# Kernel tuning notes

Hardware: AMD Instinct MI355X
Metric: run time of the kernel (lower is better)

The kernel has to match this reference:

```python
import jax, jax.numpy as jnp
import numpy as np

BERT_DIM = 768
N_ROWS = 5
N_COLS = 12
LN_EPS = 1e-5


def setup_inputs() -> dict:
    key = jax.random.key(0)
    ks = jax.random.split(key, 12)
    B, S = 256, 512
    token_hidden = jax.random.normal(ks[0], (B, S, BERT_DIM), dtype=jnp.float32)
    attention_mask = jax.random.randint(ks[1], (B, S), 0, 2, dtype=jnp.int32)
    s = lambda fan_in: 1.0 / np.sqrt(fan_in)
    return {
        "token_hidden": token_hidden,
        "attention_mask": attention_mask,
        # token_attention: Linear(768,128) -> Tanh -> Linear(128,1)
        "att_w1": jax.random.normal(ks[2], (128, BERT_DIM), dtype=jnp.float32) * s(BERT_DIM),
        "att_b1": jnp.zeros((128,), dtype=jnp.float32),
        "att_w2": jax.random.normal(ks[3], (1, 128), dtype=jnp.float32) * s(128),
        "att_b2": jnp.zeros((1,), dtype=jnp.float32),
        # feature_projector: Linear(768,256) -> GELU -> Dropout(eval) -> Linear(256,5)
        "proj_w1": jax.random.normal(ks[4], (256, BERT_DIM), dtype=jnp.float32) * s(BERT_DIM),
        "proj_b1": jnp.zeros((256,), dtype=jnp.float32),
        "proj_w2": jax.random.normal(ks[5], (N_ROWS, 256), dtype=jnp.float32) * s(256),
        "proj_b2": jnp.zeros((N_ROWS,), dtype=jnp.float32),
        # LayerNorm([5, 12])
        "ln_gamma": jnp.ones((N_ROWS, N_COLS), dtype=jnp.float32),
        "ln_beta": jnp.zeros((N_ROWS, N_COLS), dtype=jnp.float32),
    }


def reference(token_hidden, attention_mask, att_w1, att_b1, att_w2, att_b2,
              proj_w1, proj_b1, proj_w2, proj_b2, ln_gamma, ln_beta):
    # token attention scores: [B, S]
    h = jnp.tanh(jnp.einsum("bsd,hd->bsh", token_hidden, att_w1) + att_b1)
    scores = (jnp.einsum("bsh,oh->bso", h, att_w2) + att_b2)[..., 0]
    scores = jnp.where(attention_mask == 0, jnp.finfo(scores.dtype).min, scores)
    weights = jax.nn.softmax(scores, axis=-1)
    # top-k token selection (indices sorted ascending to preserve order)
    k = min(N_COLS, token_hidden.shape[1])
    _, top_idx = jax.lax.top_k(weights, k)  # [B, k]
    top_idx = jnp.sort(top_idx, axis=-1)
    selected = jnp.take_along_axis(token_hidden, top_idx[:, :, None], axis=1)  # [B, k, D]
    # feature projector (dropout is eval no-op)
    f = jax.nn.gelu(jnp.einsum("bkd,hd->bkh", selected, proj_w1) + proj_b1, approximate=False)
    f = jnp.einsum("bkh,rh->bkr", f, proj_w2) + proj_b2  # [B, k, n_rows]
    features = jnp.transpose(f, (0, 2, 1))  # [B, n_rows, k]
    if features.shape[-1] < N_COLS:
        features = jnp.pad(features, ((0, 0), (0, 0), (0, N_COLS - features.shape[-1])))
    # LayerNorm over trailing [n_rows, n_cols]
    mean = jnp.mean(features, axis=(-2, -1), keepdims=True)
    var = jnp.var(features, axis=(-2, -1), keepdims=True)
    return ln_gamma * (features - mean) * jax.lax.rsqrt(var + LN_EPS) + ln_beta
```

## Files before the change

kernel.cpp:

```cpp
#include <hip/hip_runtime.h>
#include <math.h>

#define B_BATCH 256
#define S_LEN   512
#define D_DIM   768
#define H_ATT   128
#define TOPK    12
#define NCAND   16
#define H_PROJ  256
#define N_ROWS  5
#define N_COLS  12

typedef __bf16 bf16x8 __attribute__((ext_vector_type(8)));
typedef float  f32x4  __attribute__((ext_vector_type(4)));

#define WS_SCORES 0
#define WS_WHI    524288
#define WS_WLO    720896
#define WS_W1Q    917504
#define WS_W1P    1310720

__global__ __launch_bounds__(256) void prep_kernel(
    const float* __restrict__ w1,
    const float* __restrict__ pw1,
    __bf16* __restrict__ whi, __bf16* __restrict__ wlo,
    float* __restrict__ w1q, float* __restrict__ w1p)
{
    int id = blockIdx.x * 256 + threadIdx.x;
    if (id < 98304) {
        int j    = id & 7;
        int lane = (id >> 3) & 63;
        int rest = id >> 9;
        int nt   = rest & 7;
        int kt   = rest >> 3;
        int n = nt * 16 + (lane & 15);
        int k = kt * 32 + (lane >> 4) * 8 + j;
        float f = w1[n * D_DIM + k];
        __bf16 h = (__bf16)f;
        whi[id] = h;
        wlo[id] = (__bf16)(f - (float)h);
    } else if (id < 196608) {
        int e2 = id - 98304;
        int i  = e2 & 3;
        int n  = (e2 >> 2) & 127;
        int k4 = e2 >> 9;
        w1q[e2] = w1[n * D_DIM + k4 * 4 + i];
    } else {
        int e  = id - 196608;
        int i  = e & 3;
        int j  = (e >> 2) & 255;
        int k4 = e >> 10;
        w1p[e] = pw1[j * D_DIM + k4 * 4 + i];
    }
}

__device__ inline void split8(float4 a, float4 b, bf16x8& hi, bf16x8& lo) {
    float v[8] = {a.x, a.y, a.z, a.w, b.x, b.y, b.z, b.w};
#pragma unroll
    for (int i = 0; i < 8; ++i) {
        __bf16 h = (__bf16)v[i];
        hi[i] = h;
        lo[i] = (__bf16)(v[i] - (float)h);
    }
}

__global__ __launch_bounds__(256, 3) void score_mfma(
    const float*  __restrict__ th,
    const __bf16* __restrict__ whi,
    const __bf16* __restrict__ wlo,
    const float*  __restrict__ b1,
    const float*  __restrict__ w2,
    float* __restrict__ scores)
{
    const int tid = threadIdx.x;
    const int wv  = tid >> 6;
    const int ln  = tid & 63;

    const size_t row0 = (size_t)blockIdx.x * 128 + wv * 32 + (ln & 15);
    const float* pa0 = th + row0 * D_DIM + (ln >> 4) * 8;
    const float* pa1 = pa0 + 16 * D_DIM;

    f32x4 acc[2][8];
    const f32x4 z = {0.f, 0.f, 0.f, 0.f};
#pragma unroll
    for (int i = 0; i < 2; ++i)
#pragma unroll
        for (int j = 0; j < 8; ++j) acc[i][j] = z;

    float4 c00 = *(const float4*)(pa0);
    float4 c01 = *(const float4*)(pa0 + 4);
    float4 c10 = *(const float4*)(pa1);
    float4 c11 = *(const float4*)(pa1 + 4);

    for (int kt = 0; kt < 24; ++kt) {
        float4 n00, n01, n10, n11;
        if (kt < 23) {
            n00 = *(const float4*)(pa0 + (kt + 1) * 32);
            n01 = *(const float4*)(pa0 + (kt + 1) * 32 + 4);
            n10 = *(const float4*)(pa1 + (kt + 1) * 32);
            n11 = *(const float4*)(pa1 + (kt + 1) * 32 + 4);
        }

        bf16x8 ah0, al0, ah1, al1;
        split8(c00, c01, ah0, al0);
        split8(c10, c11, ah1, al1);

        const __bf16* ph = whi + (size_t)kt * 4096 + (size_t)ln * 8;
        const __bf16* pl = wlo + (size_t)kt * 4096 + (size_t)ln * 8;
#pragma unroll
        for (int nt = 0; nt < 8; ++nt) {
            bf16x8 bh = *(const bf16x8*)(ph + nt * 512);
            bf16x8 bl = *(const bf16x8*)(pl + nt * 512);
            acc[0][nt] = __builtin_amdgcn_mfma_f32_16x16x32_bf16(ah0, bh, acc[0][nt], 0, 0, 0);
            acc[0][nt] = __builtin_amdgcn_mfma_f32_16x16x32_bf16(al0, bh, acc[0][nt], 0, 0, 0);
            acc[0][nt] = __builtin_amdgcn_mfma_f32_16x16x32_bf16(ah0, bl, acc[0][nt], 0, 0, 0);
            acc[1][nt] = __builtin_amdgcn_mfma_f32_16x16x32_bf16(ah1, bh, acc[1][nt], 0, 0, 0);
            acc[1][nt] = __builtin_amdgcn_mfma_f32_16x16x32_bf16(al1, bh, acc[1][nt], 0, 0, 0);
            acc[1][nt] = __builtin_amdgcn_mfma_f32_16x16x32_bf16(ah1, bl, acc[1][nt], 0, 0, 0);
        }
        if (kt < 23) {
            c00 = n00; c01 = n01; c10 = n10; c11 = n11;
        }
    }

    const int col = ln & 15;
    float b1v[8], w2v[8];
#pragma unroll
    for (int nt = 0; nt < 8; ++nt) {
        b1v[nt] = b1[nt * 16 + col];
        w2v[nt] = w2[nt * 16 + col];
    }
    const size_t rowbase = (size_t)blockIdx.x * 128 + wv * 32;
#pragma unroll
    for (int mf = 0; mf < 2; ++mf)
#pragma unroll
        for (int r = 0; r < 4; ++r) {
            float s = 0.f;
#pragma unroll
            for (int nt = 0; nt < 8; ++nt)
                s += tanhf(acc[mf][nt][r] + b1v[nt]) * w2v[nt];
            s += __shfl_xor(s, 1, 64);
            s += __shfl_xor(s, 2, 64);
            s += __shfl_xor(s, 4, 64);
            s += __shfl_xor(s, 8, 64);
            if (col == 0)
                scores[rowbase + mf * 16 + (ln >> 4) * 4 + r] = s;
        }
}

__global__ __launch_bounds__(256) void select_kernel(
    const float* __restrict__ th,
    const int*   __restrict__ mask,
    const float* __restrict__ ascores,
    const float* __restrict__ w1q,
    const float* __restrict__ ab1,
    const float* __restrict__ aw2,
    const float* __restrict__ w1p,
    const float* __restrict__ pb1,
    const float* __restrict__ pw2,
    const float* __restrict__ pb2,
    const float* __restrict__ gamma,
    const float* __restrict__ beta,
    float* __restrict__ out)
{
    const int b   = blockIdx.x;
    const int tid = threadIdx.x;
    const int wv  = tid >> 6;
    const int ln  = tid & 63;

    __shared__ float4 xc[NCAND][192];
    __shared__ unsigned long long wtop[64];
    __shared__ int   cand[NCAND];
    __shared__ float redW[4][8];
    __shared__ float exact_sc[NCAND];
    __shared__ int   sel_slot[TOPK];
    __shared__ float gbuf[TOPK][H_PROJ + 4];
    __shared__ float feat[N_ROWS * N_COLS];
    __shared__ float stats[2];

    const float NEG_MIN = -3.402823466e38f;

    {
        int i0 = wv * 128 + ln, i1 = i0 + 64;
        float v0 = ascores[(size_t)b * S_LEN + i0];
        if (mask[(size_t)b * S_LEN + i0] == 0) v0 = NEG_MIN;
        float v1 = ascores[(size_t)b * S_LEN + i1];
        if (mask[(size_t)b * S_LEN + i1] == 0) v1 = NEG_MIN;
        unsigned k0 = __float_as_uint(v0);
        k0 = ((int)k0 >= 0) ? (k0 | 0x80000000u) : ~k0;
        unsigned k1 = __float_as_uint(v1);
        k1 = ((int)k1 >= 0) ? (k1 | 0x80000000u) : ~k1;
        unsigned long long p0 = ((unsigned long long)k0 << 32) | (0xFFFFFFFFu - (unsigned)i0);
        unsigned long long p1 = ((unsigned long long)k1 << 32) | (0xFFFFFFFFu - (unsigned)i1);
        for (int it = 0; it < NCAND; ++it) {
            unsigned long long m = p0 > p1 ? p0 : p1;
#pragma unroll
            for (int s = 1; s <= 32; s <<= 1) {
                unsigned long long o = __shfl_xor(m, s, 64);
                if (o > m) m = o;
            }
            if (ln == 0) wtop[wv * 16 + it] = m;
            if (p0 == m) p0 = 0ull;
            else if (p1 == m) p1 = 0ull;
        }
    }
    __syncthreads();
    if (wv == 0) {
        unsigned long long q = wtop[ln];
        for (int it = 0; it < NCAND; ++it) {
            unsigned long long m = q;
#pragma unroll
            for (int s = 1; s <= 32; s <<= 1) {
                unsigned long long o = __shfl_xor(m, s, 64);
                if (o > m) m = o;
            }
            if (ln == 0) cand[it] = (int)(0xFFFFFFFFu - (unsigned)(m & 0xFFFFFFFFu));
            if (q == m) q = 0ull;
        }
    }
    __syncthreads();

#pragma unroll
    for (int i = 0; i < 12; ++i) {
        int f = tid + 256 * i;
        int c = f / 192, k4 = f % 192;
        xc[c][k4] = *(const float4*)(th + ((size_t)b * S_LEN + cand[c]) * D_DIM + k4 * 4);
    }
    __syncthreads();

    {
        const int n = tid & 127;
        const int h = tid >> 7;
        float accs[8];
#pragma unroll
        for (int ci = 0; ci < 8; ++ci) accs[ci] = 0.f;
        for (int k4 = 0; k4 < 192; ++k4) {
            float4 w = *(const float4*)(w1q + (size_t)(k4 * 128 + n) * 4);
#pragma unroll
            for (int ci = 0; ci < 8; ++ci) {
                float4 x = xc[2 * ci + h][k4];
                accs[ci] += w.x * x.x + w.y * x.y + w.z * x.z + w.w * x.w;
            }
        }
        float b1n = ab1[n], w2n = aw2[n];
#pragma unroll
        for (int ci = 0; ci < 8; ++ci) {
            float val = tanhf(accs[ci] + b1n) * w2n;
            val += __shfl_xor(val, 1, 64);
            val += __shfl_xor(val, 2, 64);
            val += __shfl_xor(val, 4, 64);
            val += __shfl_xor(val, 8, 64);
            val += __shfl_xor(val, 16, 64);
            val += __shfl_xor(val, 32, 64);
            if (ln == 0) redW[wv][ci] = val;
        }
    }
    __syncthreads();
    if (tid < NCAND) {
        int c = tid;
        float ex = (c & 1) ? (redW[2][c >> 1] + redW[3][c >> 1])
                           : (redW[0][c >> 1] + redW[1][c >> 1]);
        if (mask[(size_t)b * S_LEN + cand[c]] == 0) ex = -INFINITY;
        exact_sc[c] = ex;
    }
    __syncthreads();

    if (tid == 0) {
        unsigned picked = 0;
        int slots[TOPK];
        for (int it = 0; it < TOPK; ++it) {
            float best = -INFINITY; int bslot = -1; int bidx = 1 << 30;
            for (int c = 0; c < NCAND; ++c) {
                if (picked & (1u << c)) continue;
                float e = exact_sc[c]; int idx = cand[c];
                if (e > best || (e == best && idx < bidx)) { best = e; bslot = c; bidx = idx; }
            }
            picked |= 1u << bslot;
            slots[it] = bslot;
        }
        for (int i = 1; i < TOPK; ++i) {
            int s = slots[i], key = cand[s], j = i - 1;
            while (j >= 0 && cand[slots[j]] > key) { slots[j + 1] = slots[j]; --j; }
            slots[j + 1] = s;
        }
        for (int t = 0; t < TOPK; ++t) sel_slot[t] = slots[t];
    }
    __syncthreads();

    {
        const int j = tid;
        int slots[TOPK];
#pragma unroll
        for (int t = 0; t < TOPK; ++t) slots[t] = sel_slot[t];
        float accp[TOPK];
        float bj = pb1[j];
#pragma unroll
        for (int t = 0; t < TOPK; ++t) accp[t] = bj;
        for (int k4 = 0; k4 < 192; ++k4) {
            float4 w = *(const float4*)(w1p + ((size_t)k4 * 256 + j) * 4);
#pragma unroll
            for (int t = 0; t < TOPK; ++t) {
                float4 x = xc[slots[t]][k4];
                accp[t] += w.x * x.x + w.y * x.y + w.z * x.z + w.w * x.w;
            }
        }
#pragma unroll
        for (int t = 0; t < TOPK; ++t) {
            float hh = accp[t];
            gbuf[t][j] = 0.5f * hh * (1.0f + erff(hh * 0.70710678118654752f));
        }
    }
    __syncthreads();

    if (tid < TOPK * N_ROWS) {
        int t = tid / N_ROWS, r = tid % N_ROWS;
        float s = pb2[r];
        const float4* gp = (const float4*)&gbuf[t][0];
        const float4* wp = (const float4*)(pw2 + r * H_PROJ);
        for (int q = 0; q < H_PROJ / 4; ++q) {
            float4 g = gp[q], w = wp[q];
            s += g.x * w.x + g.y * w.y + g.z * w.z + g.w * w.w;
        }
        feat[r * N_COLS + t] = s;
    }
    __syncthreads();

    if (tid == 0) {
        float sum = 0.f;
        for (int i = 0; i < N_ROWS * N_COLS; ++i) sum += feat[i];
        float mean = sum / 60.f;
        float sq = 0.f;
        for (int i = 0; i < N_ROWS * N_COLS; ++i) { float d = feat[i] - mean; sq += d * d; }
        stats[0] = mean;
        stats[1] = sq / 60.f;
    }
    __syncthreads();
    if (tid < N_ROWS * N_COLS) {
        float x = feat[tid];
        out[(size_t)b * 60 + tid] =
            gamma[tid] * (x - stats[0]) * rsqrtf(stats[1] + 1e-5f) + beta[tid];
    }
}

extern "C" void kernel_launch(void* const* d_in, const int* in_sizes, int n_in,
                              void* d_out, int out_size, void* d_ws, size_t ws_size,
                              hipStream_t stream) {
    const float* th   = (const float*)d_in[0];
    const int*   mask = (const int*)  d_in[1];
    const float* aw1  = (const float*)d_in[2];
    const float* ab1  = (const float*)d_in[3];
    const float* aw2  = (const float*)d_in[4];
    const float* pw1  = (const float*)d_in[6];
    const float* pb1  = (const float*)d_in[7];
    const float* pw2  = (const float*)d_in[8];
    const float* pb2  = (const float*)d_in[9];
    const float* gam  = (const float*)d_in[10];
    const float* bet  = (const float*)d_in[11];
    float* out = (float*)d_out;

    char* ws = (char*)d_ws;
    float*  scores = (float*)(ws + WS_SCORES);
    __bf16* whi    = (__bf16*)(ws + WS_WHI);
    __bf16* wlo    = (__bf16*)(ws + WS_WLO);
    float*  w1q    = (float*)(ws + WS_W1Q);
    float*  w1p    = (float*)(ws + WS_W1P);

    hipLaunchKernelGGL(prep_kernel, dim3(1536), dim3(256), 0, stream,
                       aw1, pw1, whi, wlo, w1q, w1p);
    hipLaunchKernelGGL(score_mfma, dim3(1024), dim3(256), 0, stream,
                       th, whi, wlo, ab1, aw2, scores);
    hipLaunchKernelGGL(select_kernel, dim3(B_BATCH), dim3(256), 0, stream,
                       th, mask, scores, w1q, ab1, aw2,
                       w1p, pb1, pw2, pb2, gam, bet, out);
}
```

Baseline: 752.7 us.

## Stage split-bf16 weight tiles into double-buffered LDS via global_load_lds

The score kernel now loads the hi/lo bf16 weight fragments once per block into a double-buffered shared-memory tile using direct global-to-LDS loads, with the next k-tile prefetched while the current one is consumed. Previously each of the four waves read the same weight fragments separately from global memory. The prep kernel's weight layout is reordered to nt-major so each staged chunk is contiguous. The cost is a block-wide barrier per k-step and 32KB of LDS, which may limit occupancy under the 3-blocks launch bound.

```diff
diff --git a/kernel.cpp b/kernel.cpp
--- a/kernel.cpp
+++ b/kernel.cpp
@@ -13,6 +13,9 @@
 
 typedef __bf16 bf16x8 __attribute__((ext_vector_type(8)));
 typedef float  f32x4  __attribute__((ext_vector_type(4)));
+
+#define GLOBAL_AS __attribute__((address_space(1)))
+#define LDS_AS    __attribute__((address_space(3)))
 
 #define WS_SCORES 0
 #define WS_WHI    524288
@@ -31,8 +34,8 @@
         int j    = id & 7;
         int lane = (id >> 3) & 63;
         int rest = id >> 9;
-        int nt   = rest & 7;
-        int kt   = rest >> 3;
+        int kt   = rest % 24;
+        int nt   = rest / 24;
         int n = nt * 16 + (lane & 15);
         int k = kt * 32 + (lane >> 4) * 8 + j;
         float f = w1[n * D_DIM + k];
@@ -72,6 +75,8 @@
     const float*  __restrict__ w2,
     float* __restrict__ scores)
 {
+    __shared__ __bf16 Bs[2][2][8 * 512];
+
     const int tid = threadIdx.x;
     const int wv  = tid >> 6;
     const int ln  = tid & 63;
@@ -79,6 +84,20 @@
     const size_t row0 = (size_t)blockIdx.x * 128 + wv * 32 + (ln & 15);
     const float* pa0 = th + row0 * D_DIM + (ln >> 4) * 8;
     const float* pa1 = pa0 + 16 * D_DIM;
+
+    auto stage = [&](int kt, int buf) {
+#pragma unroll
+        for (int q = 0; q < 4; ++q) {
+            int s  = wv + q * 4;
+            int hl = s >> 3;
+            int nt = s & 7;
+            const __bf16* src = (hl ? wlo : whi) +
+                                (((size_t)nt * 24 + kt) * 64 + ln) * 8;
+            __bf16* dst = &Bs[buf][hl][nt * 512];
+            __builtin_amdgcn_global_load_lds(
+                (GLOBAL_AS const void*)src, (LDS_AS void*)dst, 16, 0, 0);
+        }
+    };
 
     f32x4 acc[2][8];
     const f32x4 z = {0.f, 0.f, 0.f, 0.f};
@@ -91,26 +110,28 @@
     float4 c01 = *(const float4*)(pa0 + 4);
     float4 c10 = *(const float4*)(pa1);
     float4 c11 = *(const float4*)(pa1 + 4);
+    stage(0, 0);
+    __syncthreads();
 
     for (int kt = 0; kt < 24; ++kt) {
+        const int buf = kt & 1;
         float4 n00, n01, n10, n11;
         if (kt < 23) {
             n00 = *(const float4*)(pa0 + (kt + 1) * 32);
             n01 = *(const float4*)(pa0 + (kt + 1) * 32 + 4);
             n10 = *(const float4*)(pa1 + (kt + 1) * 32);
             n11 = *(const float4*)(pa1 + (kt + 1) * 32 + 4);
+            stage(kt + 1, buf ^ 1);
         }
 
         bf16x8 ah0, al0, ah1, al1;
         split8(c00, c01, ah0, al0);
         split8(c10, c11, ah1, al1);
 
-        const __bf16* ph = whi + (size_t)kt * 4096 + (size_t)ln * 8;
-        const __bf16* pl = wlo + (size_t)kt * 4096 + (size_t)ln * 8;
 #pragma unroll
         for (int nt = 0; nt < 8; ++nt) {
-            bf16x8 bh = *(const bf16x8*)(ph + nt * 512);
-            bf16x8 bl = *(const bf16x8*)(pl + nt * 512);
+            bf16x8 bh = *(bf16x8*)(&Bs[buf][0][nt * 512 + ln * 8]);
+            bf16x8 bl = *(bf16x8*)(&Bs[buf][1][nt * 512 + ln * 8]);
             acc[0][nt] = __builtin_amdgcn_mfma_f32_16x16x32_bf16(ah0, bh, acc[0][nt], 0, 0, 0);
             acc[0][nt] = __builtin_amdgcn_mfma_f32_16x16x32_bf16(al0, bh, acc[0][nt], 0, 0, 0);
             acc[0][nt] = __builtin_amdgcn_mfma_f32_16x16x32_bf16(ah0, bl, acc[0][nt], 0, 0, 0);
@@ -120,6 +141,7 @@
         }
         if (kt < 23) {
             c00 = n00; c01 = n01; c10 = n10; c11 = n11;
+            __syncthreads();
         }
     }
 
```

New measurement: 726.1 us. 1.04x faster.

## Fuse score GEMM, top-k selection and projection into one per-batch kernel

Applied to the files above, without the earlier changes.

Removes the weight prep kernel and the separate MFMA score kernel, and computes attention scores inside a single per-batch kernel with 512 threads that keeps scores in shared memory. Weights are now read in their original row-major layout and split into bf16 hi/lo inside the MFMA loop, instead of being pre-swizzled. This drops two launches and the global round trip for scores. In exchange only 256 blocks run the heavy score GEMM (fewer blocks than the previous 1024), weight loads become strided and uncoalesced, and the per-iteration weight splitting adds ALU work and register pressure.

```diff
diff --git a/kernel.cpp b/kernel.cpp
--- a/kernel.cpp
+++ b/kernel.cpp
@@ -14,46 +14,6 @@
 typedef __bf16 bf16x8 __attribute__((ext_vector_type(8)));
 typedef float  f32x4  __attribute__((ext_vector_type(4)));
 
-#define WS_SCORES 0
-#define WS_WHI    524288
-#define WS_WLO    720896
-#define WS_W1Q    917504
-#define WS_W1P    1310720
-
-__global__ __launch_bounds__(256) void prep_kernel(
-    const float* __restrict__ w1,
-    const float* __restrict__ pw1,
-    __bf16* __restrict__ whi, __bf16* __restrict__ wlo,
-    float* __restrict__ w1q, float* __restrict__ w1p)
-{
-    int id = blockIdx.x * 256 + threadIdx.x;
-    if (id < 98304) {
-        int j    = id & 7;
-        int lane = (id >> 3) & 63;
-        int rest = id >> 9;
-        int nt   = rest & 7;
-        int kt   = rest >> 3;
-        int n = nt * 16 + (lane & 15);
-        int k = kt * 32 + (lane >> 4) * 8 + j;
-        float f = w1[n * D_DIM + k];
-        __bf16 h = (__bf16)f;
-        whi[id] = h;
-        wlo[id] = (__bf16)(f - (float)h);
-    } else if (id < 196608) {
-        int e2 = id - 98304;
-        int i  = e2 & 3;
-        int n  = (e2 >> 2) & 127;
-        int k4 = e2 >> 9;
-        w1q[e2] = w1[n * D_DIM + k4 * 4 + i];
-    } else {
-        int e  = id - 196608;
-        int i  = e & 3;
-        int j  = (e >> 2) & 255;
-        int k4 = e >> 10;
-        w1p[e] = pw1[j * D_DIM + k4 * 4 + i];
-    }
-}
-
 __device__ inline void split8(float4 a, float4 b, bf16x8& hi, bf16x8& lo) {
     float v[8] = {a.x, a.y, a.z, a.w, b.x, b.y, b.z, b.w};
 #pragma unroll
@@ -64,98 +24,13 @@
     }
 }
 
-__global__ __launch_bounds__(256, 3) void score_mfma(
-    const float*  __restrict__ th,
-    const __bf16* __restrict__ whi,
-    const __bf16* __restrict__ wlo,
-    const float*  __restrict__ b1,
-    const float*  __restrict__ w2,
-    float* __restrict__ scores)
-{
-    const int tid = threadIdx.x;
-    const int wv  = tid >> 6;
-    const int ln  = tid & 63;
-
-    const size_t row0 = (size_t)blockIdx.x * 128 + wv * 32 + (ln & 15);
-    const float* pa0 = th + row0 * D_DIM + (ln >> 4) * 8;
-    const float* pa1 = pa0 + 16 * D_DIM;
-
-    f32x4 acc[2][8];
-    const f32x4 z = {0.f, 0.f, 0.f, 0.f};
-#pragma unroll
-    for (int i = 0; i < 2; ++i)
-#pragma unroll
-        for (int j = 0; j < 8; ++j) acc[i][j] = z;
-
-    float4 c00 = *(const float4*)(pa0);
-    float4 c01 = *(const float4*)(pa0 + 4);
-    float4 c10 = *(const float4*)(pa1);
-    float4 c11 = *(const float4*)(pa1 + 4);
-
-    for (int kt = 0; kt < 24; ++kt) {
-        float4 n00, n01, n10, n11;
-        if (kt < 23) {
-            n00 = *(const float4*)(pa0 + (kt + 1) * 32);
-            n01 = *(const float4*)(pa0 + (kt + 1) * 32 + 4);
-            n10 = *(const float4*)(pa1 + (kt + 1) * 32);
-            n11 = *(const float4*)(pa1 + (kt + 1) * 32 + 4);
-        }
-
-        bf16x8 ah0, al0, ah1, al1;
-        split8(c00, c01, ah0, al0);
-        split8(c10, c11, ah1, al1);
-
-        const __bf16* ph = whi + (size_t)kt * 4096 + (size_t)ln * 8;
-        const __bf16* pl = wlo + (size_t)kt * 4096 + (size_t)ln * 8;
-#pragma unroll
-        for (int nt = 0; nt < 8; ++nt) {
-            bf16x8 bh = *(const bf16x8*)(ph + nt * 512);
-            bf16x8 bl = *(const bf16x8*)(pl + nt * 512);
-            acc[0][nt] = __builtin_amdgcn_mfma_f32_16x16x32_bf16(ah0, bh, acc[0][nt], 0, 0, 0);
-            acc[0][nt] = __builtin_amdgcn_mfma_f32_16x16x32_bf16(al0, bh, acc[0][nt], 0, 0, 0);
-            acc[0][nt] = __builtin_amdgcn_mfma_f32_16x16x32_bf16(ah0, bl, acc[0][nt], 0, 0, 0);
-            acc[1][nt] = __builtin_amdgcn_mfma_f32_16x16x32_bf16(ah1, bh, acc[1][nt], 0, 0, 0);
-            acc[1][nt] = __builtin_amdgcn_mfma_f32_16x16x32_bf16(al1, bh, acc[1][nt], 0, 0, 0);
-            acc[1][nt] = __builtin_amdgcn_mfma_f32_16x16x32_bf16(ah1, bl, acc[1][nt], 0, 0, 0);
-        }
-        if (kt < 23) {
-            c00 = n00; c01 = n01; c10 = n10; c11 = n11;
-        }
-    }
-
-    const int col = ln & 15;
-    float b1v[8], w2v[8];
-#pragma unroll
-    for (int nt = 0; nt < 8; ++nt) {
-        b1v[nt] = b1[nt * 16 + col];
-        w2v[nt] = w2[nt * 16 + col];
-    }
-    const size_t rowbase = (size_t)blockIdx.x * 128 + wv * 32;
-#pragma unroll
-    for (int mf = 0; mf < 2; ++mf)
-#pragma unroll
-        for (int r = 0; r < 4; ++r) {
-            float s = 0.f;
-#pragma unroll
-            for (int nt = 0; nt < 8; ++nt)
-                s += tanhf(acc[mf][nt][r] + b1v[nt]) * w2v[nt];
-            s += __shfl_xor(s, 1, 64);
-            s += __shfl_xor(s, 2, 64);
-            s += __shfl_xor(s, 4, 64);
-            s += __shfl_xor(s, 8, 64);
-            if (col == 0)
-                scores[rowbase + mf * 16 + (ln >> 4) * 4 + r] = s;
-        }
-}
-
-__global__ __launch_bounds__(256) void select_kernel(
+__global__ __launch_bounds__(512, 2) void fused_kernel(
     const float* __restrict__ th,
     const int*   __restrict__ mask,
-    const float* __restrict__ ascores,
-    const float* __restrict__ w1q,
+    const float* __restrict__ aw1,
     const float* __restrict__ ab1,
     const float* __restrict__ aw2,
-    const float* __restrict__ w1p,
+    const float* __restrict__ pw1,
     const float* __restrict__ pb1,
     const float* __restrict__ pw2,
     const float* __restrict__ pb2,
@@ -168,10 +43,11 @@
     const int wv  = tid >> 6;
     const int ln  = tid & 63;
 
+    __shared__ float score_s[S_LEN];
     __shared__ float4 xc[NCAND][192];
-    __shared__ unsigned long long wtop[64];
+    __shared__ unsigned long long wtop[128];
     __shared__ int   cand[NCAND];
-    __shared__ float redW[4][8];
+    __shared__ float redW[8][4];
     __shared__ float exact_sc[NCAND];
     __shared__ int   sel_slot[TOPK];
     __shared__ float gbuf[TOPK][H_PROJ + 4];
@@ -180,20 +56,111 @@
 
     const float NEG_MIN = -3.402823466e38f;
 
+    const int col = ln & 15;
+    const int kq  = ln >> 4;
+
+    for (int g = 0; g < 2; ++g) {
+        const size_t row0 = (size_t)b * S_LEN + g * 256 + wv * 32 + col;
+        const float* pa0 = th + row0 * D_DIM + kq * 8;
+        const float* pa1 = pa0 + 16 * D_DIM;
+
+        f32x4 acc[2][8];
+        const f32x4 z = {0.f, 0.f, 0.f, 0.f};
+#pragma unroll
+        for (int i = 0; i < 2; ++i)
+#pragma unroll
+            for (int j = 0; j < 8; ++j) acc[i][j] = z;
+
+        float4 c00 = *(const float4*)(pa0);
+        float4 c01 = *(const float4*)(pa0 + 4);
+        float4 c10 = *(const float4*)(pa1);
+        float4 c11 = *(const float4*)(pa1 + 4);
+        float4 bc[8][2];
+#pragma unroll
+        for (int nt = 0; nt < 8; ++nt) {
+            const float* pb = aw1 + (size_t)(nt * 16 + col) * D_DIM + kq * 8;
+            bc[nt][0] = *(const float4*)(pb);
+            bc[nt][1] = *(const float4*)(pb + 4);
+        }
+
+        for (int kt = 0; kt < 24; ++kt) {
+            float4 n00, n01, n10, n11;
+            float4 bn[8][2];
+            if (kt < 23) {
+                n00 = *(const float4*)(pa0 + (kt + 1) * 32);
+                n01 = *(const float4*)(pa0 + (kt + 1) * 32 + 4);
+                n10 = *(const float4*)(pa1 + (kt + 1) * 32);
+                n11 = *(const float4*)(pa1 + (kt + 1) * 32 + 4);
+#pragma unroll
+                for (int nt = 0; nt < 8; ++nt) {
+                    const float* pb = aw1 + (size_t)(nt * 16 + col) * D_DIM +
+                                      (kt + 1) * 32 + kq * 8;
+                    bn[nt][0] = *(const float4*)(pb);
+                    bn[nt][1] = *(const float4*)(pb + 4);
+                }
+            }
+
+            bf16x8 ah0, al0, ah1, al1;
+            split8(c00, c01, ah0, al0);
+            split8(c10, c11, ah1, al1);
+
+#pragma unroll
+            for (int nt = 0; nt < 8; ++nt) {
+                bf16x8 bh, bl;
+                split8(bc[nt][0], bc[nt][1], bh, bl);
+                acc[0][nt] = __builtin_amdgcn_mfma_f32_16x16x32_bf16(ah0, bh, acc[0][nt], 0, 0, 0);
+                acc[0][nt] = __builtin_amdgcn_mfma_f32_16x16x32_bf16(al0, bh, acc[0][nt], 0, 0, 0);
+                acc[0][nt] = __builtin_amdgcn_mfma_f32_16x16x32_bf16(ah0, bl, acc[0][nt], 0, 0, 0);
+                acc[1][nt] = __builtin_amdgcn_mfma_f32_16x16x32_bf16(ah1, bh, acc[1][nt], 0, 0, 0);
+                acc[1][nt] = __builtin_amdgcn_mfma_f32_16x16x32_bf16(al1, bh, acc[1][nt], 0, 0, 0);
+                acc[1][nt] = __builtin_amdgcn_mfma_f32_16x16x32_bf16(ah1, bl, acc[1][nt], 0, 0, 0);
+            }
+
+            if (kt < 23) {
+                c00 = n00; c01 = n01; c10 = n10; c11 = n11;
+#pragma unroll
+                for (int nt = 0; nt < 8; ++nt) {
+                    bc[nt][0] = bn[nt][0];
+                    bc[nt][1] = bn[nt][1];
+                }
+            }
+        }
+
+        float b1v[8], w2v[8];
+#pragma unroll
+        for (int nt = 0; nt < 8; ++nt) {
+            b1v[nt] = ab1[nt * 16 + col];
+            w2v[nt] = aw2[nt * 16 + col];
+        }
+        const int rowbase = g * 256 + wv * 32;
+#pragma unroll
+        for (int mf = 0; mf < 2; ++mf)
+#pragma unroll
+            for (int r = 0; r < 4; ++r) {
+                float s = 0.f;
+#pragma unroll
+                for (int nt = 0; nt < 8; ++nt)
+                    s += tanhf(acc[mf][nt][r] + b1v[nt]) * w2v[nt];
+                s += __shfl_xor(s, 1, 64);
+                s += __shfl_xor(s, 2, 64);
+                s += __shfl_xor(s, 4, 64);
+                s += __shfl_xor(s, 8, 64);
+                if (col == 0)
+                    score_s[rowbase + mf * 16 + kq * 4 + r] = s;
+            }
+    }
+    __syncthreads();
+
     {
-        int i0 = wv * 128 + ln, i1 = i0 + 64;
-        float v0 = ascores[(size_t)b * S_LEN + i0];
+        int i0 = wv * 64 + ln;
+        float v0 = score_s[i0];
         if (mask[(size_t)b * S_LEN + i0] == 0) v0 = NEG_MIN;
-        float v1 = ascores[(size_t)b * S_LEN + i1];
-        if (mask[(size_t)b * S_LEN + i1] == 0) v1 = NEG_MIN;
         unsigned k0 = __float_as_uint(v0);
         k0 = ((int)k0 >= 0) ? (k0 | 0x80000000u) : ~k0;
-        unsigned k1 = __float_as_uint(v1);
-        k1 = ((int)k1 >= 0) ? (k1 | 0x80000000u) : ~k1;
-        unsigned long long p0 = ((unsigned long long)k0 << 32) | (0xFFFFFFFFu - (unsigned)i0);
-        unsigned long long p1 = ((unsigned long long)k1 << 32) | (0xFFFFFFFFu - (unsigned)i1);
+        unsigned long long p0 =
+            ((unsigned long long)k0 << 32) | (0xFFFFFFFFu - (unsigned)i0);
         for (int it = 0; it < NCAND; ++it) {
-            unsigned long long m = p0 > p1 ? p0 : p1;
+            unsigned long long m = p0;
 #pragma unroll
             for (int s = 1; s <= 32; s <<= 1) {
                 unsigned long long o = __shfl_xor(m, s, 64);
@@ -201,28 +168,29 @@
             }
             if (ln == 0) wtop[wv * 16 + it] = m;
             if (p0 == m) p0 = 0ull;
-            else if (p1 == m) p1 = 0ull;
         }
     }
     __syncthreads();
     if (wv == 0) {
-        unsigned long long q = wtop[ln];
+        unsigned long long p0 = wtop[ln];
+        unsigned long long p1 = wtop[64 + ln];
         for (int it = 0; it < NCAND; ++it) {
-            unsigned long long m = q;
+            unsigned long long m = p0 > p1 ? p0 : p1;
 #pragma unroll
             for (int s = 1; s <= 32; s <<= 1) {
                 unsigned long long o = __shfl_xor(m, s, 64);
                 if (o > m) m = o;
             }
             if (ln == 0) cand[it] = (int)(0xFFFFFFFFu - (unsigned)(m & 0xFFFFFFFFu));
-            if (q == m) q = 0ull;
-        }
-    }
-    __syncthreads();
-
-#pragma unroll
-    for (int i = 0; i < 12; ++i) {
-        int f = tid + 256 * i;
+            if (p0 == m) p0 = 0ull;
+            else if (p1 == m) p1 = 0ull;
+        }
+    }
+    __syncthreads();
+
+#pragma unroll
+    for (int i = 0; i < 6; ++i) {
+        int f = tid + 512 * i;
         int c = f / 192, k4 = f % 192;
         xc[c][k4] = *(const float4*)(th + ((size_t)b * S_LEN + cand[c]) * D_DIM + k4 * 4);
     }
@@ -231,35 +199,33 @@
     {
         const int n = tid & 127;
         const int h = tid >> 7;
-        float accs[8];
-#pragma unroll
-        for (int ci = 0; ci < 8; ++ci) accs[ci] = 0.f;
+        float accs[4] = {0.f, 0.f, 0.f, 0.f};
+        const float* wrow = aw1 + (size_t)n * D_DIM;
         for (int k4 = 0; k4 < 192; ++k4) {
-            float4 w = *(const float4*)(w1q + (size_t)(k4 * 128 + n) * 4);
-#pragma unroll
-            for (int ci = 0; ci < 8; ++ci) {
-                float4 x = xc[2 * ci + h][k4];
-                accs[ci] += w.x * x.x + w.y * x.y + w.z * x.z + w.w * x.w;
+            float4 w = *(const float4*)(wrow + k4 * 4);
+#pragma unroll
+            for (int j = 0; j < 4; ++j) {
+                float4 x = xc[4 * h + j][k4];
+                accs[j] += w.x * x.x + w.y * x.y + w.z * x.z + w.w * x.w;
             }
         }
         float b1n = ab1[n], w2n = aw2[n];
 #pragma unroll
-        for (int ci = 0; ci < 8; ++ci) {
-            float val = tanhf(accs[ci] + b1n) * w2n;
+        for (int j = 0; j < 4; ++j) {
+            float val = tanhf(accs[j] + b1n) * w2n;
             val += __shfl_xor(val, 1, 64);
             val += __shfl_xor(val, 2, 64);
             val += __shfl_xor(val, 4, 64);
             val += __shfl_xor(val, 8, 64);
             val += __shfl_xor(val, 16, 64);
             val += __shfl_xor(val, 32, 64);
-            if (ln == 0) redW[wv][ci] = val;
+            if (ln == 0) redW[wv][j] = val;
         }
     }
     __syncthreads();
     if (tid < NCAND) {
-        int c = tid;
-        float ex = (c & 1) ? (redW[2][c >> 1] + redW[3][c >> 1])
-                           : (redW[0][c >> 1] + redW[1][c >> 1]);
+        int c = tid, h = c >> 2, j = c & 3;
+        float ex = redW[2 * h][j] + redW[2 * h + 1][j];
         if (mask[(size_t)b * S_LEN + cand[c]] == 0) ex = -INFINITY;
         exact_sc[c] = ex;
     }
@@ -288,26 +254,28 @@
     __syncthreads();
 
     {
-        const int j = tid;
-        int slots[TOPK];
-#pragma unroll
-        for (int t = 0; t < TOPK; ++t) slots[t] = sel_slot[t];
-        float accp[TOPK];
+        const int j  = tid & 255;
+        const int hh = tid >> 8;
+        int slots[6];
+#pragma unroll
+        for (int t = 0; t < 6; ++t) slots[t] = sel_slot[hh * 6 + t];
+        float accp[6];
         float bj = pb1[j];
 #pragma unroll
-        for (int t = 0; t < TOPK; ++t) accp[t] = bj;
+        for (int t = 0; t < 6; ++t) accp[t] = bj;
+        const float* wrow = pw1 + (size_t)j * D_DIM;
         for (int k4 = 0; k4 < 192; ++k4) {
-            float4 w = *(const float4*)(w1p + ((size_t)k4 * 256 + j) * 4);
-#pragma unroll
-            for (int t = 0; t < TOPK; ++t) {
+            float4 w = *(const float4*)(wrow + k4 * 4);
+#pragma unroll
+            for (int t = 0; t < 6; ++t) {
                 float4 x = xc[slots[t]][k4];
                 accp[t] += w.x * x.x + w.y * x.y + w.z * x.z + w.w * x.w;
             }
         }
 #pragma unroll
-        for (int t = 0; t < TOPK; ++t) {
-            float hh = accp[t];
-            gbuf[t][j] = 0.5f * hh * (1.0f + erff(hh * 0.70710678118654752f));
+        for (int t = 0; t < 6; ++t) {
+            float hv = accp[t];
+            gbuf[hh * 6 + t][j] = 0.5f * hv * (1.0f + erff(hv * 0.70710678118654752f));
         }
     }
     __syncthreads();
@@ -358,18 +326,9 @@
     const float* bet  = (const float*)d_in[11];
     float* out = (float*)d_out;
 
-    char* ws = (char*)d_ws;
-    float*  scores = (float*)(ws + WS_SCORES);
-    __bf16* whi    = (__bf16*)(ws + WS_WHI);
-    __bf16* wlo    = (__bf16*)(ws + WS_WLO);
-    float*  w1q    = (float*)(ws + WS_W1Q);
-    float*  w1p    = (float*)(ws + WS_W1P);
-
-    hipLaunchKernelGGL(prep_kernel, dim3(1536), dim3(256), 0, stream,
-                       aw1, pw1, whi, wlo, w1q, w1p);
-    hipLaunchKernelGGL(score_mfma, dim3(1024), dim3(256), 0, stream,
-                       th, whi, wlo, ab1, aw2, scores);
-    hipLaunchKernelGGL(select_kernel, dim3(B_BATCH), dim3(256), 0, stream,
-                       th, mask, scores, w1q, ab1, aw2,
-                       w1p, pb1, pw2, pb2, gam, bet, out);
+    (void)d_ws; (void)ws_size;
+
+    hipLaunchKernelGGL(fused_kernel, dim3(B_BATCH), dim3(512), 0, stream,
+                       th, mask, aw1, ab1, aw2, pw1, pb1, pw2, pb2,
+                       gam, bet, out);
 }
```

After: 788.4 us. 1.05x slower.
